# Performance work log

Hardware: AMD Instinct MI355X
Metric: run time of the kernel (lower is better)

The kernel has to match this reference:

```python
import jax, jax.numpy as jnp
import numpy as np

EPS = float(np.finfo(np.float32).eps)
FFT_SIZE, HOP, WIN = 1024, 120, 600
ANCHOR, KF = 7, 7
LRELU_SLOPE = 0.1

def make_log_shift(anchor=ANCHOR, kf=KF, out_scale=1000.0, in_scale=0.001):
    s = (np.arange(kf) + 1) / anchor
    ls = out_scale * np.log(in_scale * s)
    ls -= ls[anchor - 1]
    return -ls  # positive, monotonically decreasing to 0 at the anchor tap

SHIFTS = make_log_shift()

def stft_mag(y):
    # y: (B, T) -> (B, 513, n_frames), matches torch.stft(center=True, reflect)
    B, T = y.shape
    pad = FFT_SIZE // 2
    yp = jnp.pad(y, ((0, 0), (pad, pad)), mode='reflect')
    n_frames = 1 + (T + 2 * pad - FFT_SIZE) // HOP
    idx = jnp.arange(n_frames)[:, None] * HOP + jnp.arange(FFT_SIZE)[None, :]
    frames = yp[:, idx]                                  # (B, n_frames, fft)
    n = np.arange(WIN)
    w = 0.5 * (1.0 - np.cos(2.0 * np.pi * n / WIN))      # periodic Hann(600)
    lp = (FFT_SIZE - WIN) // 2                           # centered pad to fft
    w = jnp.asarray(np.pad(w, (lp, FFT_SIZE - WIN - lp)), dtype=y.dtype)
    spec = jnp.fft.rfft(frames * w, axis=-1)
    mag = jnp.sqrt(jnp.clip(spec.real ** 2 + spec.imag ** 2, EPS))
    return jnp.transpose(mag, (0, 2, 1))

def int_shift(x, k):
    # output[..., f, :] = x[..., f-k, :], zero-fill; k >= 0 (static python int)
    F = x.shape[2]
    if k == 0:
        return x
    if k >= F:
        return jnp.zeros_like(x)
    return jnp.pad(x[:, :, :F - k, :], ((0, 0), (0, 0), (k, 0), (0, 0)))

def frac_shift(x, s):
    # linear-interpolation frequency shift (= interp_shift CUDA kernel)
    if s == int(s):
        return int_shift(x, int(s))
    s0 = int(np.floor(s)); frac = float(s - s0)
    return (1.0 - frac) * int_shift(x, s0) + frac * int_shift(x, s0 + 1)

def wnorm(v, g):
    # weight_norm: w = g * v / ||v|| (norm over all dims but out-channel)
    n = jnp.sqrt(jnp.sum(v * v, axis=(1, 2, 3), keepdims=True))
    return g * v / n

def conv2d(x, w, b, stride, padding):
    out = jax.lax.conv_general_dilated(
        x, w, window_strides=stride,
        padding=((padding[0], padding[0]), (padding[1], padding[1])),
        dimension_numbers=('NCHW', 'OIHW', 'NCHW'))
    return out + b[None, :, None, None]

def lrelu(x):
    return jax.nn.leaky_relu(x, LRELU_SLOPE)

def harmonic_conv(x, v, g, b):
    # x: (B,1,F,T). Log-harmonic lowering: stack 7 fractionally-shifted copies
    lowered = jnp.concatenate([frac_shift(x, SHIFTS[fk]) for fk in range(KF)], axis=1)
    w = wnorm(v, g)                                      # (32, 7, 1, 7)
    return conv2d(lowered, w, b, (1, 1), (0, 3))         # padding[0] forced to 0

def setup_inputs() -> dict:
    key = jax.random.key(0)
    ks = jax.random.split(key, 16)
    p = {}
    p['y'] = jax.random.normal(ks[0], (4, 1, 96000), dtype=jnp.float32)
    p['v0'] = jax.random.normal(ks[1], (32, 7, 1, 7), dtype=jnp.float32) * 0.05
    p['g0'] = jnp.ones((32, 1, 1, 1), dtype=jnp.float32)
    p['b0'] = jnp.zeros((32,), dtype=jnp.float32)
    for i, kk in zip((1, 2, 3), (2, 3, 4)):
        p[f'v{i}'] = jax.random.normal(ks[kk], (32, 32, 3, 9), dtype=jnp.float32) * 0.05
        p[f'g{i}'] = jnp.ones((32, 1, 1, 1), dtype=jnp.float32)
        p[f'b{i}'] = jnp.zeros((32,), dtype=jnp.float32)
    p['v4'] = jax.random.normal(ks[5], (32, 32, 3, 3), dtype=jnp.float32) * 0.05
    p['g4'] = jnp.ones((32, 1, 1, 1), dtype=jnp.float32)
    p['b4'] = jnp.zeros((32,), dtype=jnp.float32)
    p['vo'] = jax.random.normal(ks[6], (1, 32, 3, 3), dtype=jnp.float32) * 0.05
    p['go'] = jnp.ones((1, 1, 1, 1), dtype=jnp.float32)
    p['bo'] = jnp.zeros((1,), dtype=jnp.float32)
    return p

def reference(y, v0, g0, b0, v1, g1, b1, v2, g2, b2, v3, g3, b3,
              v4, g4, b4, vo, go, bo):
    mag = stft_mag(y[:, 0, :])          # (B, 513, frames)
    x = mag[:, None]                    # (B, 1, 513, frames)
    fmap = []
    x = lrelu(harmonic_conv(x, v0, g0, b0)); fmap.append(x)
    x = lrelu(conv2d(x, wnorm(v1, g1), b1, (1, 2), (1, 4))); fmap.append(x)
    x = lrelu(conv2d(x, wnorm(v2, g2), b2, (1, 2), (1, 4))); fmap.append(x)
    x = lrelu(conv2d(x, wnorm(v3, g3), b3, (1, 2), (1, 4))); fmap.append(x)
    x = lrelu(conv2d(x, wnorm(v4, g4), b4, (1, 1), (1, 1))); fmap.append(x)
    x = conv2d(x, wnorm(vo, go), bo, (1, 1), (1, 1)); fmap.append(x)
    flat = x.reshape(x.shape[0], -1)
    return (flat,) + tuple(fmap)
```

## Files before the change

kernel.cpp:

```cpp
#include <hip/hip_runtime.h>
#include <math.h>

#define T_SAMPLES 96000
#define NFRAMES 801
#define NBINS 513
#define EPS32 1.1920928955078125e-07f

typedef _Float16 f16;
typedef f16 f16x2 __attribute__((ext_vector_type(2)));
typedef f16 f16x4 __attribute__((ext_vector_type(4)));
typedef f16 f16x8 __attribute__((ext_vector_type(8)));
typedef float f32x4 __attribute__((ext_vector_type(4)));
typedef float f32x16 __attribute__((ext_vector_type(16)));

__global__ __launch_bounds__(512) void stft_kernel(const float* __restrict__ y,
                                                   float* __restrict__ mag)
{
    int t = blockIdx.x;
    int b = blockIdx.y;
    int tid = threadIdx.x;

    __shared__ float2 buf[2][1024];

    const float* yb = y + (size_t)b * T_SAMPLES;
    for (int n = tid; n < 1024; n += 512) {
        int j = t * 120 + n - 512;
        if (j < 0) j = -j;
        if (j >= T_SAMPLES) j = 2 * T_SAMPLES - 2 - j;
        float v = yb[j];
        int np_ = n - 212;
        float w = 0.0f;
        if (np_ >= 0 && np_ < 600)
            w = 0.5f * (1.0f - cospif((float)np_ * (1.0f / 300.0f)));
        buf[0][n] = make_float2(v * w, 0.0f);
    }
    __syncthreads();

    int srcb = 0;
    #pragma unroll
    for (int stage = 0; stage < 10; ++stage) {
        int m  = 1 << stage;
        int jm = (tid >> stage) << stage;
        float jf = (float)jm * (1.0f / 512.0f);
        float wr = cospif(jf);
        float wi = -sinpif(jf);
        float2 a  = buf[srcb][tid];
        float2 bb = buf[srcb][tid + 512];
        float2 s  = make_float2(a.x + bb.x, a.y + bb.y);
        float2 d  = make_float2(a.x - bb.x, a.y - bb.y);
        float2 dw = make_float2(d.x * wr - d.y * wi, d.x * wi + d.y * wr);
        buf[srcb ^ 1][tid + jm]     = s;
        buf[srcb ^ 1][tid + jm + m] = dw;
        __syncthreads();
        srcb ^= 1;
    }

    float2 v = buf[srcb][tid];
    float msq = v.x * v.x + v.y * v.y;
    mag[((size_t)b * NBINS + tid) * NFRAMES + t] = sqrtf(fmaxf(msq, EPS32));
    if (tid == 0) {
        float2 v5 = buf[srcb][512];
        float m5 = v5.x * v5.x + v5.y * v5.y;
        mag[((size_t)b * NBINS + 512) * NFRAMES + t] = sqrtf(fmaxf(m5, EPS32));
    }
}

__global__ __launch_bounds__(256) void prep_kernel(
    const float* __restrict__ v0, const float* __restrict__ g0,
    const float* __restrict__ v1, const float* __restrict__ g1,
    const float* __restrict__ v2, const float* __restrict__ g2,
    const float* __restrict__ v3, const float* __restrict__ g3,
    const float* __restrict__ v4, const float* __restrict__ g4,
    const float* __restrict__ vo, const float* __restrict__ go,
    float* __restrict__ w0n, float* __restrict__ won,
    f16* __restrict__ A1, f16* __restrict__ A2,
    f16* __restrict__ A3, f16* __restrict__ A4)
{
    int blk = blockIdx.x;
    int tid = threadIdx.x;

    const float *v, *g; f16* Ap = nullptr; float* outf = nullptr;
    int o, per_o, KW = 9;
    if (blk < 32)        { v = v1; g = g1; Ap = A1; o = blk;       per_o = 864; }
    else if (blk < 64)   { v = v2; g = g2; Ap = A2; o = blk - 32;  per_o = 864; }
    else if (blk < 96)   { v = v3; g = g3; Ap = A3; o = blk - 64;  per_o = 864; }
    else if (blk < 128)  { v = v4; g = g4; Ap = A4; o = blk - 96;  per_o = 288; KW = 3; }
    else if (blk < 160)  { v = v0; g = g0; outf = w0n; o = blk - 128; per_o = 49; }
    else                 { v = vo; g = go; outf = won; o = 0;        per_o = 288; }

    const float* vv = v + (size_t)o * per_o;
    __shared__ float red[256];
    float s = 0.f;
    for (int i = tid; i < per_o; i += 256) { float x = vv[i]; s = fmaf(x, x, s); }
    red[tid] = s;
    __syncthreads();
    for (int k = 128; k > 0; k >>= 1) {
        if (tid < k) red[tid] += red[tid + k];
        __syncthreads();
    }
    float scale = g[o] / sqrtf(red[0]);

    if (outf) {
        for (int i = tid; i < per_o; i += 256)
            outf[(size_t)o * per_o + i] = vv[i] * scale;
    } else {
        for (int i = tid; i < per_o; i += 256) {
            int tap = i >> 5;
            int c   = i & 31;
            int df  = tap / KW, kw = tap - df * KW;
            float val = vv[(c * 3 + df) * KW + kw] * scale;
            int l = ((c >> 3) & 1) * 32 + o;
            int ch = c >> 4;
            int j = c & 7;
            Ap[(((tap * 2 + ch) * 64 + l) << 3) + j] = (f16)val;
        }
    }
}

__global__ __launch_bounds__(256) void harmonic_kernel(const float* __restrict__ mag,
                                                       const float* __restrict__ wn,
                                                       const float* __restrict__ bias,
                                                       float* __restrict__ out,
                                                       f16* __restrict__ f0c,
                                                       float fr4, float fr5)
{
    int f = blockIdx.x;
    int b = blockIdx.y;
    int tid = threadIdx.x;

    __shared__ float rows[3][808];

    const float* mb = mag + (size_t)b * NBINS * NFRAMES;

    for (int i = tid; i < 808; i += 256) {
        int tt = i - 3;
        bool ok = (tt >= 0) && (tt < NFRAMES);
        float m336 = (ok && f >= 336) ? mb[(size_t)(f - 336) * NFRAMES + tt] : 0.f;
        float m337 = (ok && f >= 337) ? mb[(size_t)(f - 337) * NFRAMES + tt] : 0.f;
        float m154 = (ok && f >= 154) ? mb[(size_t)(f - 154) * NFRAMES + tt] : 0.f;
        float m155 = (ok && f >= 155) ? mb[(size_t)(f - 155) * NFRAMES + tt] : 0.f;
        float m0   = ok ? mb[(size_t)f * NFRAMES + tt] : 0.f;
        rows[0][i] = (1.f - fr4) * m336 + fr4 * m337;
        rows[1][i] = (1.f - fr5) * m154 + fr5 * m155;
        rows[2][i] = m0;
    }
    __syncthreads();

    char* crow = (char*)f0c + ((size_t)(b * NBINS + f)) * 904 * 64;

    if (tid < 16) {
        int tg = tid >> 2, q = tid & 3;
        int swz = (((tg >> 1) & 3) << 4) | (((tg >> 3) & 1) << 6);
        f16x8 z;
        #pragma unroll
        for (int j = 0; j < 8; ++j) z[j] = (f16)0.f;
        *reinterpret_cast<f16x8*>(crow + ((tg * 64 + q * 16) ^ swz)) = z;
    }

    #pragma unroll
    for (int chunk = 0; chunk < 4; ++chunk) {
        int t = chunk * 256 + tid;
        if (t < NFRAMES) {
            float win[3][7];
            #pragma unroll
            for (int r = 0; r < 3; ++r)
                #pragma unroll
                for (int k = 0; k < 7; ++k)
                    win[r][k] = rows[r][t + k];

            float vals[32];
            #pragma unroll
            for (int o = 0; o < 32; ++o) {
                float a = bias[o];
                #pragma unroll
                for (int r = 0; r < 3; ++r) {
                    const float* wr = wn + (o * 7 + 4 + r) * 7;
                    #pragma unroll
                    for (int kw = 0; kw < 7; ++kw)
                        a = fmaf(win[r][kw], wr[kw], a);
                }
                vals[o] = (a > 0.f) ? a : 0.1f * a;
            }

            #pragma unroll
            for (int o = 0; o < 32; ++o)
                out[(((size_t)b * 32 + o) * NBINS + f) * (size_t)NFRAMES + t] = vals[o];

            int tg = t + 4;
            int swz = (((tg >> 1) & 3) << 4) | (((tg >> 3) & 1) << 6);
            #pragma unroll
            for (int q = 0; q < 4; ++q) {
                f16x8 h;
                #pragma unroll
                for (int j = 0; j < 8; ++j) h[j] = (f16)vals[q * 8 + j];
                *reinterpret_cast<f16x8*>(crow + ((tg * 64 + q * 16) ^ swz)) = h;
            }
        } else if (t < 900) {
            int tg = t + 4;
            int swz = (((tg >> 1) & 3) << 4) | (((tg >> 3) & 1) << 6);
            f16x8 z;
            #pragma unroll
            for (int j = 0; j < 8; ++j) z[j] = (f16)0.f;
            #pragma unroll
            for (int q = 0; q < 4; ++q)
                *reinterpret_cast<f16x8*>(crow + ((tg * 64 + q * 16) ^ swz)) = z;
        }
    }
}

template<int KW, int STRIDE, int PW, int PAD_IN, int PAD_OUT, bool DO_LRELU>
__global__ __launch_bounds__(256, 3) void conv_v3(
    const float* __restrict__ inF, const f16* __restrict__ inC,
    const f16* __restrict__ Ap, const float* __restrict__ bias,
    float* __restrict__ out, f16* __restrict__ outC,
    int Tin, int Tout, int TpadIn, int TpadOut)
{
    constexpr int NT    = 64;
    constexpr int TR    = NT * STRIDE + KW - 1;
    constexpr int TRP   = (TR + 1) & ~1;
    constexpr int ROWB  = TRP * 64;
    constexpr int TOFF  = PAD_IN ? ((PAD_IN - PW) & 15) : 0;
    constexpr int NFOFF = 32 * STRIDE * 64;

    __shared__ char ldsb[6 * TRP * 64];

    const int tid  = threadIdx.x;
    const int lane = tid & 63;
    const int wave = tid >> 6;
    const int t0   = blockIdx.x * NT;
    const int f0   = blockIdx.y * 4;
    const int b    = blockIdx.z;
    const int tbase = t0 * STRIDE - PW;

    if constexpr (PAD_IN == 0) {
        constexpr int NSTG = 6 * 16 * TRP;
        const float* inb = inF + (size_t)b * 32 * NBINS * Tin;
        for (int i = tid; i < NSTG; i += 256) {
            int trow = i % TRP;
            int cf   = i / TRP;
            int cp   = (cf & 15) << 1;
            int fr   = cf >> 4;
            int fi = f0 - 1 + fr;
            int ti = tbase + trow;
            float va = 0.f, vb = 0.f;
            if (fi >= 0 && fi < NBINS && ti >= 0 && ti < Tin) {
                const float* p = inb + ((size_t)cp * NBINS + fi) * Tin + ti;
                va = p[0];
                vb = p[(size_t)NBINS * Tin];
            }
            f16x2 h; h[0] = (f16)va; h[1] = (f16)vb;
            int byte = fr * ROWB + trow * 64 + cp * 2;
            byte ^= ((trow >> 1) & 3) << 4;
            byte ^= ((trow >> 3) & 1) << 6;
            *reinterpret_cast<f16x2*>(ldsb + byte) = h;
        }
    } else {
        constexpr int SL = TRP * 4;
        constexpr int NS = 6 * SL;
        const int g0 = tbase + PAD_IN;
        #pragma unroll
        for (int it = 0; it < (NS + 255) / 256; ++it) {
            int slot = tid + it * 256;
            if (slot < NS) {
                int fr = slot / SL;
                int s  = slot - fr * SL;
                int fi = f0 - 1 + fr;
                f16x8 v;
                if (fi >= 0 && fi < NBINS) {
                    size_t idx = (((size_t)(b * NBINS + fi)) * TpadIn + g0) * 32 + (size_t)s * 8;
                    v = *reinterpret_cast<const f16x8*>(inC + idx);
                } else {
                    #pragma unroll
                    for (int j = 0; j < 8; ++j) v[j] = (f16)0.f;
                }
                *reinterpret_cast<f16x8*>(ldsb + slot * 16) = v;
            }
        }
    }

    const int tln = lane & 31;
    const int hi  = lane >> 5;
    int baddr0[KW];
    #pragma unroll
    for (int kw = 0; kw < KW; ++kw) {
        int trow = tln * STRIDE + kw;
        int x = trow + TOFF;
        int swz = (((x >> 1) & 3) << 4) | (((x >> 3) & 1) << 6);
        baddr0[kw] = (trow * 64 + hi * 16) ^ swz;
    }

    __syncthreads();

    f32x16 acc[2];
    #pragma unroll
    for (int nf = 0; nf < 2; ++nf)
        #pragma unroll
        for (int r = 0; r < 16; ++r) acc[nf][r] = 0.f;

    const char* lrow = ldsb + wave * ROWB;
    #pragma unroll
    for (int df = 0; df < 3; ++df) {
        f16x8 a[KW * 2];
        #pragma unroll
        for (int kw = 0; kw < KW; ++kw)
            #pragma unroll
            for (int ch = 0; ch < 2; ++ch)
                a[kw * 2 + ch] = *reinterpret_cast<const f16x8*>(
                    Ap + (((df * KW + kw) * 2 + ch) << 9) + lane * 8);
        #pragma unroll
        for (int kw = 0; kw < KW; ++kw) {
            #pragma unroll
            for (int ch = 0; ch < 2; ++ch) {
                #pragma unroll
                for (int nf = 0; nf < 2; ++nf) {
                    f16x8 bf = *reinterpret_cast<const f16x8*>(
                        lrow + ((baddr0[kw] ^ (ch << 5)) + df * ROWB + nf * NFOFF));
                    acc[nf] = __builtin_amdgcn_mfma_f32_32x32x16_f16(a[kw * 2 + ch], bf, acc[nf], 0, 0, 0);
                }
            }
        }
    }

    const int f = f0 + wave;
    if (f >= NBINS) return;

    float bs[16];
    #pragma unroll
    for (int r = 0; r < 16; ++r)
        bs[r] = bias[4 * hi + 8 * (r >> 2) + (r & 3)];

    char* crow = nullptr;
    if constexpr (PAD_OUT > 0)
        crow = (char*)outC + ((size_t)(b * NBINS + f)) * TpadOut * 64;

    #pragma unroll
    for (int nf = 0; nf < 2; ++nf) {
        int t = t0 + nf * 32 + tln;
        bool vt = (t < Tout);
        float vals[16];
        #pragma unroll
        for (int r = 0; r < 16; ++r) {
            float v = acc[nf][r] + bs[r];
            if (DO_LRELU) v = (v > 0.f) ? v : 0.1f * v;
            vals[r] = v;
        }
        if (vt) {
            #pragma unroll
            for (int r = 0; r < 16; ++r) {
                int o = 4 * hi + 8 * (r >> 2) + (r & 3);
                out[(((size_t)b * 32 + o) * NBINS + f) * Tout + t] = vals[r];
            }
        }
        if constexpr (PAD_OUT > 0) {
            int tg = t + PAD_OUT;
            int swz = (((tg >> 1) & 3) << 4) | (((tg >> 3) & 1) << 6);
            int rowbyte = (tg * 64) ^ swz;
            #pragma unroll
            for (int q = 0; q < 4; ++q) {
                f16x4 hv;
                if (vt) {
                    #pragma unroll
                    for (int r = 0; r < 4; ++r) hv[r] = (f16)vals[4 * q + r];
                } else {
                    #pragma unroll
                    for (int r = 0; r < 4; ++r) hv[r] = (f16)0.f;
                }
                int byte = rowbyte ^ ((4 * hi + 8 * q) << 1);
                *reinterpret_cast<f16x4*>(crow + byte) = hv;
            }
        }
    }
    if constexpr (PAD_OUT > 0) {
        if (blockIdx.x == 0 && lane < PAD_OUT * 4) {
            int tgp = lane >> 2, oct = lane & 3;
            f16x8 z;
            #pragma unroll
            for (int j = 0; j < 8; ++j) z[j] = (f16)0.f;
            *reinterpret_cast<f16x8*>(crow + tgp * 64 + oct * 16) = z;
        }
    }
}

__global__ __launch_bounds__(256) void convo_kernel(const float* __restrict__ in,
                                                    const float* __restrict__ wn,
                                                    const float* __restrict__ bias,
                                                    float* __restrict__ f5,
                                                    float* __restrict__ flat)
{
    int idx = blockIdx.x * 256 + threadIdx.x;
    if (idx >= 4 * NBINS * 101) return;
    int t = idx % 101;
    int rem = idx / 101;
    int f = rem % NBINS;
    int b = rem / NBINS;

    float a = bias[0];
    const float* inb = in + (size_t)b * 32 * NBINS * 101;
    for (int c = 0; c < 32; ++c) {
        #pragma unroll
        for (int df = 0; df < 3; ++df) {
            int fi = f + df - 1;
            if (fi < 0 || fi >= NBINS) continue;
            #pragma unroll
            for (int kw = 0; kw < 3; ++kw) {
                int ti = t + kw - 1;
                if (ti < 0 || ti >= 101) continue;
                a = fmaf(inb[((size_t)c * NBINS + fi) * 101 + ti], wn[(c * 3 + df) * 3 + kw], a);
            }
        }
    }
    f5[idx] = a;
    flat[idx] = a;
}

extern "C" void kernel_launch(void* const* d_in, const int* in_sizes, int n_in,
                              void* d_out, int out_size, void* d_ws, size_t ws_size,
                              hipStream_t stream)
{
    const float* y  = (const float*)d_in[0];
    const float* v0 = (const float*)d_in[1];
    const float* g0 = (const float*)d_in[2];
    const float* b0 = (const float*)d_in[3];
    const float* v1 = (const float*)d_in[4];
    const float* g1 = (const float*)d_in[5];
    const float* b1 = (const float*)d_in[6];
    const float* v2 = (const float*)d_in[7];
    const float* g2 = (const float*)d_in[8];
    const float* b2 = (const float*)d_in[9];
    const float* v3 = (const float*)d_in[10];
    const float* g3 = (const float*)d_in[11];
    const float* b3 = (const float*)d_in[12];
    const float* v4 = (const float*)d_in[13];
    const float* g4 = (const float*)d_in[14];
    const float* b4 = (const float*)d_in[15];
    const float* vo = (const float*)d_in[16];
    const float* go = (const float*)d_in[17];
    const float* bo = (const float*)d_in[18];

    float* out = (float*)d_out;
    float* ws  = (float*)d_ws;

    const size_t SFLAT = (size_t)4 * NBINS * 101;
    const size_t NF0   = (size_t)4 * 32 * NBINS * 801;
    const size_t NF1   = (size_t)4 * 32 * NBINS * 401;
    const size_t NF2   = (size_t)4 * 32 * NBINS * 201;
    const size_t NF3   = (size_t)4 * 32 * NBINS * 101;
    float* oflat = out;
    float* f0 = out + SFLAT;
    float* f1 = f0 + NF0;
    float* f2 = f1 + NF1;
    float* f3 = f2 + NF2;
    float* f4 = f3 + NF3;
    float* f5 = f4 + NF3;

    float* mag = f1;

    size_t off = 0;
    float* w0n = ws + off; off += 1568;
    float* won = ws + off; off += 288;
    f16* A1 = (f16*)(ws + off);
    f16* A2 = A1 + 27648;
    f16* A3 = A2 + 27648;
    f16* A4 = A3 + 27648;
    f16* f0c = A4 + 9216;
    const int TP0 = 904;
    f16* f1c = f0c + (size_t)4 * NBINS * TP0 * 32;
    const int TP1 = 520;
    f16* f2c = f1c + (size_t)4 * NBINS * TP1 * 32;
    const int TP2 = 264;
    f16* f3c = f2c + (size_t)4 * NBINS * TP2 * 32;
    const int TP3 = 136;

    prep_kernel<<<161, 256, 0, stream>>>(v0, g0, v1, g1, v2, g2, v3, g3,
                                         v4, g4, vo, go, w0n, won,
                                         A1, A2, A3, A4);

    stft_kernel<<<dim3(NFRAMES, 4), 512, 0, stream>>>(y, mag);

    double sh4 = -(1000.0 * log(0.001 * (5.0 / 7.0)) - 1000.0 * log(0.001));
    double sh5 = -(1000.0 * log(0.001 * (6.0 / 7.0)) - 1000.0 * log(0.001));
    float fr4 = (float)(sh4 - floor(sh4));
    float fr5 = (float)(sh5 - floor(sh5));

    harmonic_kernel<<<dim3(NBINS, 4), 256, 0, stream>>>(mag, w0n, b0, f0, f0c, fr4, fr5);

    conv_v3<9, 2, 4, 4, 4, true><<<dim3(7, 129, 4), 256, 0, stream>>>(
        nullptr, f0c, A1, b1, f1, f1c, 801, 401, TP0, TP1);
    conv_v3<9, 2, 4, 4, 4, true><<<dim3(4, 129, 4), 256, 0, stream>>>(
        nullptr, f1c, A2, b2, f2, f2c, 401, 201, TP1, TP2);
    conv_v3<9, 2, 4, 4, 5, true><<<dim3(2, 129, 4), 256, 0, stream>>>(
        nullptr, f2c, A3, b3, f3, f3c, 201, 101, TP2, TP3);
    conv_v3<3, 1, 1, 5, 0, true><<<dim3(2, 129, 4), 256, 0, stream>>>(
        nullptr, f3c, A4, b4, f4, nullptr, 101, 101, TP3, 0);

    convo_kernel<<<(int)((4 * NBINS * 101 + 255) / 256), 256, 0, stream>>>(f4, won, bo, f5, oflat);
}
```

Baseline: 461.7 us.

## Make conv kernels persistent over time tiles with double-buffered LDS staging and guard rows

Replaces conv_v3 with conv_v4. Each workgroup owns one (batch, 4-frequency) block and loops over 32-wide time tiles. The global loads for the next tile are prefetched into registers and committed to a second LDS buffer while the current tile runs its MFMAs. Workgroup IDs are remapped so that consecutive blocks land on the same XCD, and the channel-last fp16 buffers gain zero guard rows above and below plus shrunk padded widths, so staging loads need no boundary branches. A new zero_pads kernel clears the guard rows and tails, which adds one launch. Occupancy drops to 2 blocks per SIMD and each tile now computes only 32 outputs per wave.

```diff
diff --git a/kernel.cpp b/kernel.cpp
--- a/kernel.cpp
+++ b/kernel.cpp
@@ -4,6 +4,7 @@
 #define T_SAMPLES 96000
 #define NFRAMES 801
 #define NBINS 513
+#define FROWS 515
 #define EPS32 1.1920928955078125e-07f
 
 typedef _Float16 f16;
@@ -65,6 +66,41 @@
     }
 }
 
+__global__ __launch_bounds__(256) void zero_pads(f16* p0, f16* p1, f16* p2, f16* p3)
+{
+    const int TPs[4]   = {840, 456, 264, 136};
+    const int tails[4] = {840, 420, 228, 133};
+    f16* ptrs[4] = {p0, p1, p2, p3};
+    int l = blockIdx.y;
+    f16* p = ptrs[l];
+    int TP = TPs[l], tail = tails[l];
+    int rowSlots   = TP * 4;
+    int guardSlots = 8 * rowSlots;
+    int tailCols   = TP - tail;
+    int tailSlots  = 4 * FROWS * tailCols * 4;
+    int total = guardSlots + tailSlots;
+    f16x8 z;
+    #pragma unroll
+    for (int j = 0; j < 8; ++j) z[j] = (f16)0.f;
+    for (int i = blockIdx.x * 256 + threadIdx.x; i < total; i += gridDim.x * 256) {
+        size_t slot;
+        if (i < guardSlots) {
+            int rs = i / rowSlots;
+            int q  = i - rs * rowSlots;
+            int b  = rs >> 1;
+            int r  = (rs & 1) ? (FROWS - 1) : 0;
+            slot = ((size_t)(b * FROWS + r)) * rowSlots + q;
+        } else {
+            int j2 = i - guardSlots;
+            int per = tailCols * 4;
+            int row = j2 / per;
+            int q   = j2 - row * per;
+            slot = ((size_t)row * TP + tail) * 4 + q;
+        }
+        *reinterpret_cast<f16x8*>((char*)p + slot * 16) = z;
+    }
+}
+
 __global__ __launch_bounds__(256) void prep_kernel(
     const float* __restrict__ v0, const float* __restrict__ g0,
     const float* __restrict__ v1, const float* __restrict__ g1,
@@ -146,7 +182,7 @@
     }
     __syncthreads();
 
-    char* crow = (char*)f0c + ((size_t)(b * NBINS + f)) * 904 * 64;
+    char* crow = (char*)f0c + ((size_t)(b * FROWS + f + 1)) * 840 * 64;
 
     if (tid < 16) {
         int tg = tid >> 2, q = tid & 3;
@@ -195,7 +231,7 @@
                 for (int j = 0; j < 8; ++j) h[j] = (f16)vals[q * 8 + j];
                 *reinterpret_cast<f16x8*>(crow + ((tg * 64 + q * 16) ^ swz)) = h;
             }
-        } else if (t < 900) {
+        } else if (t < 836) {
             int tg = t + 4;
             int swz = (((tg >> 1) & 3) << 4) | (((tg >> 3) & 1) << 6);
             f16x8 z;
@@ -208,75 +244,65 @@
     }
 }
 
-template<int KW, int STRIDE, int PW, int PAD_IN, int PAD_OUT, bool DO_LRELU>
-__global__ __launch_bounds__(256, 3) void conv_v3(
-    const float* __restrict__ inF, const f16* __restrict__ inC,
-    const f16* __restrict__ Ap, const float* __restrict__ bias,
-    float* __restrict__ out, f16* __restrict__ outC,
-    int Tin, int Tout, int TpadIn, int TpadOut)
-{
-    constexpr int NT    = 64;
-    constexpr int TR    = NT * STRIDE + KW - 1;
-    constexpr int TRP   = (TR + 1) & ~1;
-    constexpr int ROWB  = TRP * 64;
-    constexpr int TOFF  = PAD_IN ? ((PAD_IN - PW) & 15) : 0;
-    constexpr int NFOFF = 32 * STRIDE * 64;
-
-    __shared__ char ldsb[6 * TRP * 64];
+template<int KW, int STRIDE, int PW, int PAD_IN, int PAD_OUT, int NTB, bool DO_LRELU>
+__global__ __launch_bounds__(256, 2) void conv_v4(
+    const f16* __restrict__ inC, const f16* __restrict__ Ap,
+    const float* __restrict__ bias, float* __restrict__ out,
+    f16* __restrict__ outC, int Tout, int TpadIn, int TpadOut)
+{
+    constexpr int NT   = 32;
+    constexpr int TR   = NT * STRIDE + KW - 1;
+    constexpr int TRP  = (TR + 1) & ~1;
+    constexpr int ROWB = TRP * 64;
+    constexpr int BUFB = 6 * ROWB;
+    constexpr int SL   = BUFB / 16;
+    constexpr int KPT  = (SL + 255) / 256;
+    constexpr int TOFF = (PAD_IN - PW) & 15;
+
+    __shared__ char ldsb[2 * BUFB];
 
     const int tid  = threadIdx.x;
     const int lane = tid & 63;
     const int wave = tid >> 6;
-    const int t0   = blockIdx.x * NT;
-    const int f0   = blockIdx.y * 4;
-    const int b    = blockIdx.z;
-    const int tbase = t0 * STRIDE - PW;
-
-    if constexpr (PAD_IN == 0) {
-        constexpr int NSTG = 6 * 16 * TRP;
-        const float* inb = inF + (size_t)b * 32 * NBINS * Tin;
-        for (int i = tid; i < NSTG; i += 256) {
-            int trow = i % TRP;
-            int cf   = i / TRP;
-            int cp   = (cf & 15) << 1;
-            int fr   = cf >> 4;
-            int fi = f0 - 1 + fr;
-            int ti = tbase + trow;
-            float va = 0.f, vb = 0.f;
-            if (fi >= 0 && fi < NBINS && ti >= 0 && ti < Tin) {
-                const float* p = inb + ((size_t)cp * NBINS + fi) * Tin + ti;
-                va = p[0];
-                vb = p[(size_t)NBINS * Tin];
-            }
-            f16x2 h; h[0] = (f16)va; h[1] = (f16)vb;
-            int byte = fr * ROWB + trow * 64 + cp * 2;
-            byte ^= ((trow >> 1) & 3) << 4;
-            byte ^= ((trow >> 3) & 1) << 6;
-            *reinterpret_cast<f16x2*>(ldsb + byte) = h;
-        }
-    } else {
-        constexpr int SL = TRP * 4;
-        constexpr int NS = 6 * SL;
-        const int g0 = tbase + PAD_IN;
+
+    const int NWG = 129 * 4;
+    int l0 = blockIdx.x;
+    int xcd = l0 & 7, sl = l0 >> 3;
+    const int q = NWG / 8, r = NWG % 8;
+    int work = (xcd < r ? xcd * (q + 1) : r * (q + 1) + (xcd - r) * q) + sl;
+    const int b    = work / 129;
+    const int fblk = work - b * 129;
+    const int f0   = fblk * 4;
+    const int brow = b * FROWS + f0;
+
+    size_t sbase[KPT];
+    #pragma unroll
+    for (int k = 0; k < KPT; ++k) {
+        int s = tid + k * 256;
+        int fr = s / (TRP * 4);
+        int s2 = s - fr * (TRP * 4);
+        sbase[k] = ((size_t)(brow + fr) * TpadIn) * 64 + (size_t)s2 * 16;
+    }
+
+    f16x8 stg[KPT];
+    const char* inB = (const char*)inC;
+
+    auto issue = [&](int tb) {
+        size_t g0b = (size_t)(tb * (NT * STRIDE) + (PAD_IN - PW)) * 64;
         #pragma unroll
-        for (int it = 0; it < (NS + 255) / 256; ++it) {
-            int slot = tid + it * 256;
-            if (slot < NS) {
-                int fr = slot / SL;
-                int s  = slot - fr * SL;
-                int fi = f0 - 1 + fr;
-                f16x8 v;
-                if (fi >= 0 && fi < NBINS) {
-                    size_t idx = (((size_t)(b * NBINS + fi)) * TpadIn + g0) * 32 + (size_t)s * 8;
-                    v = *reinterpret_cast<const f16x8*>(inC + idx);
-                } else {
-                    #pragma unroll
-                    for (int j = 0; j < 8; ++j) v[j] = (f16)0.f;
-                }
-                *reinterpret_cast<f16x8*>(ldsb + slot * 16) = v;
-            }
-        }
-    }
+        for (int k = 0; k < KPT; ++k) {
+            if (KPT * 256 == SL || tid + k * 256 < SL)
+                stg[k] = *reinterpret_cast<const f16x8*>(inB + sbase[k] + g0b);
+        }
+    };
+    auto commit = [&](int bufsel) {
+        #pragma unroll
+        for (int k = 0; k < KPT; ++k) {
+            int s = tid + k * 256;
+            if (KPT * 256 == SL || s < SL)
+                *reinterpret_cast<f16x8*>(ldsb + bufsel * BUFB + s * 16) = stg[k];
+        }
+    };
 
     const int tln = lane & 31;
     const int hi  = lane >> 5;
@@ -289,95 +315,90 @@
         baddr0[kw] = (trow * 64 + hi * 16) ^ swz;
     }
 
+    float bs[16];
+    #pragma unroll
+    for (int rr = 0; rr < 16; ++rr) bs[rr] = bias[4 * hi + 8 * (rr >> 2) + (rr & 3)];
+
+    const int f = f0 + wave;
+    char* crow = nullptr;
+    if constexpr (PAD_OUT > 0)
+        crow = (char*)outC + ((size_t)(b * FROWS + f + 1)) * TpadOut * 64;
+
+    issue(0);
+    commit(0);
     __syncthreads();
-
-    f32x16 acc[2];
-    #pragma unroll
-    for (int nf = 0; nf < 2; ++nf)
+    int cur = 0;
+
+    #pragma unroll 1
+    for (int tb = 0; tb < NTB; ++tb) {
+        if (tb + 1 < NTB) issue(tb + 1);
+
+        f32x16 acc;
         #pragma unroll
-        for (int r = 0; r < 16; ++r) acc[nf][r] = 0.f;
-
-    const char* lrow = ldsb + wave * ROWB;
-    #pragma unroll
-    for (int df = 0; df < 3; ++df) {
-        f16x8 a[KW * 2];
+        for (int rr = 0; rr < 16; ++rr) acc[rr] = 0.f;
+
+        const char* lbase = ldsb + cur * BUFB + wave * ROWB;
         #pragma unroll
-        for (int kw = 0; kw < KW; ++kw)
-            #pragma unroll
-            for (int ch = 0; ch < 2; ++ch)
-                a[kw * 2 + ch] = *reinterpret_cast<const f16x8*>(
-                    Ap + (((df * KW + kw) * 2 + ch) << 9) + lane * 8);
-        #pragma unroll
-        for (int kw = 0; kw < KW; ++kw) {
-            #pragma unroll
-            for (int ch = 0; ch < 2; ++ch) {
-                #pragma unroll
-                for (int nf = 0; nf < 2; ++nf) {
+        for (int df = 0; df < 3; ++df) {
+            f16x8 a[KW * 2];
+            #pragma unroll
+            for (int kw = 0; kw < KW; ++kw)
+                #pragma unroll
+                for (int ch = 0; ch < 2; ++ch)
+                    a[kw * 2 + ch] = *reinterpret_cast<const f16x8*>(
+                        Ap + (((df * KW + kw) * 2 + ch) << 9) + lane * 8);
+            #pragma unroll
+            for (int kw = 0; kw < KW; ++kw)
+                #pragma unroll
+                for (int ch = 0; ch < 2; ++ch) {
                     f16x8 bf = *reinterpret_cast<const f16x8*>(
-                        lrow + ((baddr0[kw] ^ (ch << 5)) + df * ROWB + nf * NFOFF));
-                    acc[nf] = __builtin_amdgcn_mfma_f32_32x32x16_f16(a[kw * 2 + ch], bf, acc[nf], 0, 0, 0);
+                        lbase + (baddr0[kw] ^ (ch << 5)) + df * ROWB);
+                    acc = __builtin_amdgcn_mfma_f32_32x32x16_f16(a[kw * 2 + ch], bf, acc, 0, 0, 0);
+                }
+        }
+
+        if (f < NBINS) {
+            int t = tb * NT + tln;
+            bool vt = (t < Tout);
+            float vals[16];
+            #pragma unroll
+            for (int rr = 0; rr < 16; ++rr) {
+                float v = acc[rr] + bs[rr];
+                if (DO_LRELU) v = (v > 0.f) ? v : 0.1f * v;
+                vals[rr] = v;
+            }
+            if (vt) {
+                #pragma unroll
+                for (int rr = 0; rr < 16; ++rr) {
+                    int o = 4 * hi + 8 * (rr >> 2) + (rr & 3);
+                    out[(((size_t)b * 32 + o) * NBINS + f) * Tout + t] = vals[rr];
                 }
             }
-        }
-    }
-
-    const int f = f0 + wave;
-    if (f >= NBINS) return;
-
-    float bs[16];
-    #pragma unroll
-    for (int r = 0; r < 16; ++r)
-        bs[r] = bias[4 * hi + 8 * (r >> 2) + (r & 3)];
-
-    char* crow = nullptr;
-    if constexpr (PAD_OUT > 0)
-        crow = (char*)outC + ((size_t)(b * NBINS + f)) * TpadOut * 64;
-
-    #pragma unroll
-    for (int nf = 0; nf < 2; ++nf) {
-        int t = t0 + nf * 32 + tln;
-        bool vt = (t < Tout);
-        float vals[16];
-        #pragma unroll
-        for (int r = 0; r < 16; ++r) {
-            float v = acc[nf][r] + bs[r];
-            if (DO_LRELU) v = (v > 0.f) ? v : 0.1f * v;
-            vals[r] = v;
-        }
-        if (vt) {
-            #pragma unroll
-            for (int r = 0; r < 16; ++r) {
-                int o = 4 * hi + 8 * (r >> 2) + (r & 3);
-                out[(((size_t)b * 32 + o) * NBINS + f) * Tout + t] = vals[r];
+            if constexpr (PAD_OUT > 0) {
+                int tg = t + PAD_OUT;
+                int swz = (((tg >> 1) & 3) << 4) | (((tg >> 3) & 1) << 6);
+                int rowbyte = (tg * 64) ^ swz;
+                #pragma unroll
+                for (int qq = 0; qq < 4; ++qq) {
+                    f16x4 hv;
+                    #pragma unroll
+                    for (int rr = 0; rr < 4; ++rr)
+                        hv[rr] = vt ? (f16)vals[4 * qq + rr] : (f16)0.f;
+                    *reinterpret_cast<f16x4*>(crow + (rowbyte ^ ((4 * hi + 8 * qq) << 1))) = hv;
+                }
+                if (tb == 0 && lane < PAD_OUT * 4) {
+                    int tgp = lane >> 2, oct = lane & 3;
+                    f16x8 z;
+                    #pragma unroll
+                    for (int j = 0; j < 8; ++j) z[j] = (f16)0.f;
+                    *reinterpret_cast<f16x8*>(crow + tgp * 64 + oct * 16) = z;
+                }
             }
         }
-        if constexpr (PAD_OUT > 0) {
-            int tg = t + PAD_OUT;
-            int swz = (((tg >> 1) & 3) << 4) | (((tg >> 3) & 1) << 6);
-            int rowbyte = (tg * 64) ^ swz;
-            #pragma unroll
-            for (int q = 0; q < 4; ++q) {
-                f16x4 hv;
-                if (vt) {
-                    #pragma unroll
-                    for (int r = 0; r < 4; ++r) hv[r] = (f16)vals[4 * q + r];
-                } else {
-                    #pragma unroll
-                    for (int r = 0; r < 4; ++r) hv[r] = (f16)0.f;
-                }
-                int byte = rowbyte ^ ((4 * hi + 8 * q) << 1);
-                *reinterpret_cast<f16x4*>(crow + byte) = hv;
-            }
-        }
-    }
-    if constexpr (PAD_OUT > 0) {
-        if (blockIdx.x == 0 && lane < PAD_OUT * 4) {
-            int tgp = lane >> 2, oct = lane & 3;
-            f16x8 z;
-            #pragma unroll
-            for (int j = 0; j < 8; ++j) z[j] = (f16)0.f;
-            *reinterpret_cast<f16x8*>(crow + tgp * 64 + oct * 16) = z;
-        }
+
+        if (tb + 1 < NTB) commit(cur ^ 1);
+        __syncthreads();
+        cur ^= 1;
     }
 }
 
@@ -455,6 +476,7 @@
 
     float* mag = f1;
 
+    const int TP0 = 840, TP1 = 456, TP2 = 264, TP3 = 136;
     size_t off = 0;
     float* w0n = ws + off; off += 1568;
     float* won = ws + off; off += 288;
@@ -463,13 +485,11 @@
     f16* A3 = A2 + 27648;
     f16* A4 = A3 + 27648;
     f16* f0c = A4 + 9216;
-    const int TP0 = 904;
-    f16* f1c = f0c + (size_t)4 * NBINS * TP0 * 32;
-    const int TP1 = 520;
-    f16* f2c = f1c + (size_t)4 * NBINS * TP1 * 32;
-    const int TP2 = 264;
-    f16* f3c = f2c + (size_t)4 * NBINS * TP2 * 32;
-    const int TP3 = 136;
+    f16* f1c = f0c + (size_t)4 * FROWS * TP0 * 32;
+    f16* f2c = f1c + (size_t)4 * FROWS * TP1 * 32;
+    f16* f3c = f2c + (size_t)4 * FROWS * TP2 * 32;
+
+    zero_pads<<<dim3(256, 4), 256, 0, stream>>>(f0c, f1c, f2c, f3c);
 
     prep_kernel<<<161, 256, 0, stream>>>(v0, g0, v1, g1, v2, g2, v3, g3,
                                          v4, g4, vo, go, w0n, won,
@@ -484,14 +504,10 @@
 
     harmonic_kernel<<<dim3(NBINS, 4), 256, 0, stream>>>(mag, w0n, b0, f0, f0c, fr4, fr5);
 
-    conv_v3<9, 2, 4, 4, 4, true><<<dim3(7, 129, 4), 256, 0, stream>>>(
-        nullptr, f0c, A1, b1, f1, f1c, 801, 401, TP0, TP1);
-    conv_v3<9, 2, 4, 4, 4, true><<<dim3(4, 129, 4), 256, 0, stream>>>(
-        nullptr, f1c, A2, b2, f2, f2c, 401, 201, TP1, TP2);
-    conv_v3<9, 2, 4, 4, 5, true><<<dim3(2, 129, 4), 256, 0, stream>>>(
-        nullptr, f2c, A3, b3, f3, f3c, 201, 101, TP2, TP3);
-    conv_v3<3, 1, 1, 5, 0, true><<<dim3(2, 129, 4), 256, 0, stream>>>(
-        nullptr, f3c, A4, b4, f4, nullptr, 101, 101, TP3, 0);
+    conv_v4<9, 2, 4, 4, 4, 13, true><<<516, 256, 0, stream>>>(f0c, A1, b1, f1, f1c, 401, TP0, TP1);
+    conv_v4<9, 2, 4, 4, 4,  7, true><<<516, 256, 0, stream>>>(f1c, A2, b2, f2, f2c, 201, TP1, TP2);
+    conv_v4<9, 2, 4, 4, 5,  4, true><<<516, 256, 0, stream>>>(f2c, A3, b3, f3, f3c, 101, TP2, TP3);
+    conv_v4<3, 1, 1, 5, 0,  4, true><<<516, 256, 0, stream>>>(f3c, A4, b4, f4, nullptr, 101, TP3, 0);
 
     convo_kernel<<<(int)((4 * NBINS * 101 + 255) / 256), 256, 0, stream>>>(f4, won, bo, f5, oflat);
 }
```

New measurement: 975.5 us. +111.3%, slower.
